# Kernel tuning notes

Hardware: AMD Instinct MI355X
Metric: run time of the kernel (lower is better)

The kernel has to match this reference:

```python
import jax, jax.numpy as jnp
import numpy as np
import math

SR = 24000
NH = 100      # num_harmonics
NF = 5        # num_formants
HID = 128
TWO_PI = 2.0 * math.pi


def conv1d(x, w, b, groups=1):
    # x: [B,C,T], w: [O, C//groups, K] (torch OIH layout), 'same' padding
    pad = (w.shape[-1] - 1) // 2
    y = jax.lax.conv_general_dilated(
        x, w, window_strides=(1,), padding=[(pad, pad)],
        dimension_numbers=('NCH', 'OIH', 'NCH'), feature_group_count=groups)
    return y + b[None, :, None]


def lrelu(x):
    return jnp.where(x >= 0, x, 0.1 * x)


def interp_linear(x, L):
    # torch F.interpolate(mode='linear', align_corners=False): x [B,C,T] -> [B,C,L]
    B, C, T = x.shape
    pos = (jnp.arange(L, dtype=x.dtype) + 0.5) * (T / L) - 0.5
    pos = jnp.clip(pos, 0.0, float(T - 1))
    lo = jnp.floor(pos).astype(jnp.int32)
    hi = jnp.minimum(lo + 1, T - 1)
    w = pos - lo.astype(x.dtype)
    return x[:, :, lo] * (1.0 - w) + x[:, :, hi] * w


def setup_inputs():
    key = jax.random.key(0)
    ks = jax.random.split(key, 30)
    ki = iter(range(30))
    def p(shape, s=0.05):
        return s * jax.random.normal(ks[next(ki)], shape, jnp.float32)
    B, T, L = 4, 500, 120000
    inp = {}
    # f0 in [80,120) Hz so actual_harmonics == num_harmonics (static shapes, see notes)
    inp['f0'] = 80.0 + 40.0 * jax.random.uniform(ks[next(ki)], (B, T), jnp.float32)
    inp['condition'] = jax.random.normal(ks[next(ki)], (B, HID, T), jnp.float32)
    # harmonic_amplitude_net params
    inp['ha_w1'] = p((HID, 1, 3));   inp['ha_b1'] = p((HID,))
    inp['ha_w2'] = p((256, HID, 1)); inp['ha_b2'] = p((256,))
    inp['ha_w3'] = p((256, 1, 3));   inp['ha_b3'] = p((256,))
    inp['ha_w4'] = p((256, 256, 1)); inp['ha_b4'] = p((256,))
    inp['ha_w5'] = p((NH, 256, 1));  inp['ha_b5'] = p((NH,))
    # formant predictor params
    inp['fm_w1'] = p((256, HID, 3));    inp['fm_b1'] = p((256,))
    inp['fm_w2'] = p((256, 256, 3));    inp['fm_b2'] = p((256,))
    inp['fm_w3'] = p((2 * NF, 256, 1)); inp['fm_b3'] = p((2 * NF,))
    # voice quality predictor params
    inp['vq_w1'] = p((128, HID, 3)); inp['vq_b1'] = p((128,))
    inp['vq_w2'] = p((64, 128, 3));  inp['vq_b2'] = p((64,))
    inp['vq_w3'] = p((3, 64, 1));    inp['vq_b3'] = p((3,))
    inp['audio_length'] = L
    return inp


def reference(f0, condition,
              ha_w1, ha_b1, ha_w2, ha_b2, ha_w3, ha_b3, ha_w4, ha_b4, ha_w5, ha_b5,
              fm_w1, fm_b1, fm_w2, fm_b2, fm_w3, fm_b3,
              vq_w1, vq_b1, vq_w2, vq_b2, vq_w3, vq_b3,
              audio_length):
    B, T = f0.shape
    L = audio_length
    # ---- harmonic_amplitude_net: (dw3 -> pw1 -> lrelu) x2 -> pw1 -> softplus ----
    a = lrelu(conv1d(conv1d(condition, ha_w1, ha_b1, groups=HID), ha_w2, ha_b2))
    a = lrelu(conv1d(conv1d(a, ha_w3, ha_b3, groups=256), ha_w4, ha_b4))
    harmonic_amplitudes = jax.nn.softplus(conv1d(a, ha_w5, ha_b5))  # [B,NH,T]
    # ---- FormantNetwork ----
    fp = conv1d(lrelu(conv1d(lrelu(conv1d(condition, fm_w1, fm_b1)), fm_w2, fm_b2)), fm_w3, fm_b3)
    ff = 200.0 + 3300.0 * jax.nn.sigmoid(fp[:, :NF])        # [B,NF,T]
    fbw = 50.0 + 150.0 * jax.nn.softplus(fp[:, NF:])        # [B,NF,T]
    hidx = jnp.arange(1, NH + 1, dtype=f0.dtype)
    hfreq = hidx[None, :, None] * f0[:, None, :]            # [B,NH,T]
    num = fbw ** 2                                          # [B,NF,T]
    den = (hfreq[:, None] - ff[:, :, None]) ** 2 + num[:, :, None]  # [B,NF,NH,T]
    res = num[:, :, None] / jnp.maximum(den, 1e-5)
    gain = jnp.prod(0.8 + 0.2 * res, axis=1)                # [B,NH,T]
    shaped = harmonic_amplitudes * gain
    # ---- VoiceQualityNetwork ----
    q = jax.nn.sigmoid(conv1d(lrelu(conv1d(lrelu(conv1d(condition, vq_w1, vq_b1)), vq_w2, vq_b2)), vq_w3, vq_b3))
    q_up = interp_linear(q, L)                              # [B,3,L]
    jitter = q_up[:, 0] * 0.05
    shimmer = q_up[:, 1] * 0.15
    breath = q_up[:, 2] * 0.3
    # ---- phase integration + harmonic bank ----
    f0_up = interp_linear(f0[:, None, :], L)[:, 0]          # [B,L]
    phase = jnp.cumsum(TWO_PI * f0_up / SR, axis=1)
    nk1, nk2, nk3 = jax.random.split(jax.random.key(42), 3)
    jphase = phase + jitter * jax.random.normal(nk1, phase.shape, phase.dtype)
    mask = (hidx[None, :, None] * f0_up[:, None, :] < SR / 2).astype(f0.dtype)  # [B,NH,L]
    amps_up = interp_linear(shaped, L)                      # [B,NH,L]
    sig = jnp.sum(amps_up * jnp.sin(jphase[:, None, :] * hidx[None, :, None]) * mask, axis=1)
    # ---- voice qualities: shimmer envelope + breath noise ----
    shim_env = 1.0 + jax.random.normal(nk2, sig.shape, sig.dtype) * shimmer
    out = sig * shim_env + jax.random.normal(nk3, sig.shape, sig.dtype) * breath
    return out
```

## Files before the change

kernel.cpp:

```cpp
#include <hip/hip_runtime.h>
#include <stdint.h>

#define B_ 4
#define T_ 500
#define L_ 120000
#define NH_ 100
#define N1_ 7500
#define N2_ 469
#define N2P_ 7504
#define N3_ 30
#define N3P_ 480
#define N4_ 2
#define N4P_ 32

#define ACT_NONE 0
#define ACT_LRELU 1
#define ACT_SOFTPLUS 2
#define ACT_SIGMOID 3

#define CH3 32
#define SXW3 132

__host__ __device__ __forceinline__ uint32_t tf_rotl(uint32_t v, int d) {
  return (v << d) | (v >> (32 - d));
}
__host__ __device__ __forceinline__ void tf_block(uint32_t k0, uint32_t k1,
                                                  uint32_t& x0, uint32_t& x1) {
  uint32_t k2 = k0 ^ k1 ^ 0x1BD11BDAu;
  x0 += k0; x1 += k1;
#define TF_R(d) x0 += x1; x1 = tf_rotl(x1, (d)); x1 ^= x0;
  TF_R(13) TF_R(15) TF_R(26) TF_R(6)   x0 += k1; x1 += k2 + 1u;
  TF_R(17) TF_R(29) TF_R(16) TF_R(24)  x0 += k2; x1 += k0 + 2u;
  TF_R(13) TF_R(15) TF_R(26) TF_R(6)   x0 += k0; x1 += k1 + 3u;
  TF_R(17) TF_R(29) TF_R(16) TF_R(24)  x0 += k1; x1 += k2 + 4u;
  TF_R(13) TF_R(15) TF_R(26) TF_R(6)   x0 += k2; x1 += k0 + 5u;
#undef TF_R
}

__device__ __forceinline__ float erfinv_xla(float x) {
  float w = -log1pf(-(x * x));
  float p;
  if (w < 5.0f) {
    w = w - 2.5f;
    p = 2.81022636e-08f;
    p = fmaf(p, w, 3.43273939e-07f);
    p = fmaf(p, w, -3.5233877e-06f);
    p = fmaf(p, w, -4.39150654e-06f);
    p = fmaf(p, w, 0.00021858087f);
    p = fmaf(p, w, -0.00125372503f);
    p = fmaf(p, w, -0.00417768164f);
    p = fmaf(p, w, 0.246640727f);
    p = fmaf(p, w, 1.50140941f);
  } else {
    w = sqrtf(w) - 3.0f;
    p = -0.000200214257f;
    p = fmaf(p, w, 0.000100950558f);
    p = fmaf(p, w, 0.00134934322f);
    p = fmaf(p, w, -0.00367342844f);
    p = fmaf(p, w, 0.00573950773f);
    p = fmaf(p, w, -0.0076224613f);
    p = fmaf(p, w, 0.00943887047f);
    p = fmaf(p, w, 1.00167406f);
    p = fmaf(p, w, 2.83297682f);
  }
  return p * x;
}

__device__ __forceinline__ float jax_normal(uint32_t k0, uint32_t k1, uint32_t e) {
  uint32_t x0 = 0u, x1 = e;
  tf_block(k0, k1, x0, x1);
  uint32_t bits = x0 ^ x1;
  float u = __uint_as_float((bits >> 9) | 0x3f800000u) - 1.0f;
  float v = __fadd_rn(__fmul_rn(u, 2.0f), -0x1.fffffep-1f);
  v = fmaxf(v, -0x1.fffffep-1f);
  return __fmul_rn((float)1.4142135623730951, erfinv_xla(v));
}

__device__ __forceinline__ float sin_acc(float xf) {
  double x = (double)xf;
  double kd = rint(x * 6.3661977236758138e-01);
  double r = fma(-kd, 1.5707963267948966e+00, x);
  r = fma(-kd, 6.1232339957367660e-17, r);
  float rf = (float)r;
  float y = rf * rf;
  float ps = fmaf(y, 2.7557319e-06f, -1.9841270e-04f);
  ps = fmaf(y, ps, 8.3333335e-03f);
  ps = fmaf(y, ps, -0.16666667f);
  float s = fmaf(rf * y, ps, rf);
  float pc = fmaf(y, -2.7557319e-07f, 2.4801587e-05f);
  pc = fmaf(y, pc, -1.3888889e-03f);
  pc = fmaf(y, pc, 4.1666668e-02f);
  pc = fmaf(y, pc, -0.5f);
  float c = fmaf(y, pc, 1.0f);
  int q = ((int)kd) & 3;
  float rs = (q & 1) ? c : s;
  return (q & 2) ? -rs : rs;
}

__device__ __forceinline__ float apply_act(float v, int act) {
  switch (act) {
    case ACT_LRELU:    return v >= 0.0f ? v : 0.1f * v;
    case ACT_SOFTPLUS: return fmaxf(v, 0.0f) + log1pf(expf(-fabsf(v)));
    case ACT_SIGMOID:  return 1.0f / (1.0f + expf(-v));
  }
  return v;
}


__device__ __forceinline__ void conv3_tile(
    const float* __restrict__ x, const float* __restrict__ w,
    const float* __restrict__ bias, float* __restrict__ y,
    int Cin, int Cout, int o0, int act, int b, int t0, float* smem) {
  float* sxf = smem;
  float* swf = smem + CH3 * SXW3;
  int tid = threadIdx.x;
  int lane = tid & 63, og = tid >> 6;
  int tl = 2 * lane;
  int t = t0 + tl;
  int obase = o0 + og * 4;
  float acc[4][2];
#pragma unroll
  for (int i = 0; i < 4; ++i) {
    float bv = (obase + i < Cout) ? bias[obase + i] : 0.0f;
    acc[i][0] = bv; acc[i][1] = bv;
  }
  float rx[17], rw[6];
  const int nch = Cin / CH3;
  auto ld = [&](int c) {
    int cb = c * CH3;
#pragma unroll
    for (int k = 0; k < 17; ++k) {
      int idx = tid + 256 * k;
      float v = 0.0f;
      if (idx < CH3 * 130) {
        int cc = idx / 130, j = idx - cc * 130;
        int tt = t0 - 1 + j;
        if (tt >= 0 && tt < T_) v = x[((size_t)b * Cin + cb + cc) * T_ + tt];
      }
      rx[k] = v;
    }
#pragma unroll
    for (int k = 0; k < 6; ++k) {
      int idx = tid + 256 * k;
      int oo = idx / 96, r = idx - oo * 96;
      rw[k] = (o0 + oo < Cout) ? w[((size_t)(o0 + oo) * Cin + cb) * 3 + r] : 0.0f;
    }
  };
  ld(0);
  for (int c = 0; c < nch; ++c) {
    __syncthreads();
#pragma unroll
    for (int k = 0; k < 17; ++k) {
      int idx = tid + 256 * k;
      if (idx < CH3 * 130) {
        int cc = idx / 130, j = idx - cc * 130;
        sxf[cc * SXW3 + j] = rx[k];
      }
    }
#pragma unroll
    for (int k = 0; k < 6; ++k) {
      int idx = tid + 256 * k;
      int oo = idx / 96, r = idx - oo * 96;
      swf[(r / 3) * 52 + oo * 3 + (r % 3)] = rw[k];
    }
    __syncthreads();
    if (c + 1 < nch) ld(c + 1);
    for (int cc = 0; cc < CH3; ++cc) {
      const float* row = sxf + cc * SXW3 + tl;
      float2 xa = *(const float2*)row;
      float2 xb = *(const float2*)(row + 2);
      const float4* wq = (const float4*)(swf + cc * 52 + og * 12);
      float4 W0 = wq[0], W1 = wq[1], W2 = wq[2];
      float wl[12] = {W0.x, W0.y, W0.z, W0.w, W1.x, W1.y, W1.z, W1.w,
                      W2.x, W2.y, W2.z, W2.w};
#pragma unroll
      for (int i = 0; i < 4; ++i) {
        float w0 = wl[3 * i], w1 = wl[3 * i + 1], w2 = wl[3 * i + 2];
        acc[i][0] = fmaf(xa.x, w0, acc[i][0]);
        acc[i][0] = fmaf(xa.y, w1, acc[i][0]);
        acc[i][0] = fmaf(xb.x, w2, acc[i][0]);
        acc[i][1] = fmaf(xa.y, w0, acc[i][1]);
        acc[i][1] = fmaf(xb.x, w1, acc[i][1]);
        acc[i][1] = fmaf(xb.y, w2, acc[i][1]);
      }
    }
  }
#pragma unroll
  for (int i = 0; i < 4; ++i) {
    int o = obase + i;
    if (o < Cout) {
      if (t < T_)     y[((size_t)b * Cout + o) * T_ + t]     = apply_act(acc[i][0], act);
      if (t + 1 < T_) y[((size_t)b * Cout + o) * T_ + t + 1] = apply_act(acc[i][1], act);
    }
  }
}

__device__ __forceinline__ void dwpw_tile(
    const float* __restrict__ x, const float* __restrict__ wd,
    const float* __restrict__ bd, const float* __restrict__ wp,
    const float* __restrict__ bp, float* __restrict__ y,
    int Cin, int Cout, int o0, int act, int b, int t0, float* smem) {
  float* sxf  = smem;
  float* swdf = smem + CH3 * SXW3;
  float* swpf = swdf + CH3 * 4;
  int tid = threadIdx.x;
  int lane = tid & 63, og = tid >> 6;
  int tl = 2 * lane;
  int t = t0 + tl;
  int obase = o0 + og * 4;
  float acc[4][2];
#pragma unroll
  for (int i = 0; i < 4; ++i) {
    float bv = (obase + i < Cout) ? bp[obase + i] : 0.0f;
    acc[i][0] = bv; acc[i][1] = bv;
  }
  float rx[17], rwp[2], rwd1 = 0.0f;
  const int nch = Cin / CH3;
  auto ld = [&](int c) {
    int cb = c * CH3;
#pragma unroll
    for (int k = 0; k < 17; ++k) {
      int idx = tid + 256 * k;
      float v = 0.0f;
      if (idx < CH3 * 130) {
        int cc = idx / 130, j = idx - cc * 130;
        int tt = t0 - 1 + j;
        if (tt >= 0 && tt < T_) v = x[((size_t)b * Cin + cb + cc) * T_ + tt];
      }
      rx[k] = v;
    }
    if (tid < CH3 * 4) {
      int cc = tid >> 2, q = tid & 3;
      rwd1 = (q < 3) ? wd[(size_t)(cb + cc) * 3 + q] : bd[cb + cc];
    }
#pragma unroll
    for (int k = 0; k < 2; ++k) {
      int idx = tid + 256 * k;
      int oo = idx >> 5, cc = idx & 31;
      rwp[k] = (o0 + oo < Cout) ? wp[(size_t)(o0 + oo) * Cin + cb + cc] : 0.0f;
    }
  };
  ld(0);
  for (int c = 0; c < nch; ++c) {
    __syncthreads();
#pragma unroll
    for (int k = 0; k < 17; ++k) {
      int idx = tid + 256 * k;
      if (idx < CH3 * 130) {
        int cc = idx / 130, j = idx - cc * 130;
        sxf[cc * SXW3 + j] = rx[k];
      }
    }
    if (tid < CH3 * 4) swdf[tid] = rwd1;
#pragma unroll
    for (int k = 0; k < 2; ++k) {
      int idx = tid + 256 * k;
      int oo = idx >> 5, cc = idx & 31;
      swpf[cc * 16 + oo] = rwp[k];
    }
    __syncthreads();
    if (c + 1 < nch) ld(c + 1);
    for (int cc = 0; cc < CH3; ++cc) {
      const float* row = sxf + cc * SXW3 + tl;
      float2 xa = *(const float2*)row;
      float2 xb = *(const float2*)(row + 2);
      float4 D = *(const float4*)(swdf + cc * 4);
      float d0 = fmaf(xa.x, D.x, fmaf(xa.y, D.y, fmaf(xb.x, D.z, D.w)));
      float d1 = fmaf(xa.y, D.x, fmaf(xb.x, D.y, fmaf(xb.y, D.z, D.w)));
      float4 Wp = *(const float4*)(swpf + cc * 16 + og * 4);
      acc[0][0] = fmaf(d0, Wp.x, acc[0][0]);
      acc[1][0] = fmaf(d0, Wp.y, acc[1][0]);
      acc[2][0] = fmaf(d0, Wp.z, acc[2][0]);
      acc[3][0] = fmaf(d0, Wp.w, acc[3][0]);
      acc[0][1] = fmaf(d1, Wp.x, acc[0][1]);
      acc[1][1] = fmaf(d1, Wp.y, acc[1][1]);
      acc[2][1] = fmaf(d1, Wp.z, acc[2][1]);
      acc[3][1] = fmaf(d1, Wp.w, acc[3][1]);
    }
  }
#pragma unroll
  for (int i = 0; i < 4; ++i) {
    int o = obase + i;
    if (o < Cout) {
      if (t < T_)     y[((size_t)b * Cout + o) * T_ + t]     = apply_act(acc[i][0], act);
      if (t + 1 < T_) y[((size_t)b * Cout + o) * T_ + t + 1] = apply_act(acc[i][1], act);
    }
  }
}

__device__ __forceinline__ void pw_stream(
    const float* __restrict__ x, const float* __restrict__ w,
    const float* __restrict__ bias, float* __restrict__ y,
    int Cin, int Cout, int o0, int act, int b, int t0, float* smem) {
  for (int idx = threadIdx.x; idx < 16 * Cin; idx += 256) {
    int oo = idx / Cin, cc = idx - oo * Cin;
    smem[cc * 16 + oo] = (o0 + oo < Cout) ? w[(size_t)(o0 + oo) * Cin + cc] : 0.0f;
  }
  __syncthreads();
  int lane = threadIdx.x & 63, og = threadIdx.x >> 6;
  int t = t0 + lane;
  int obase = o0 + og * 4;
  float acc[4];
#pragma unroll
  for (int i = 0; i < 4; ++i)
    acc[i] = (obase + i < Cout) ? bias[obase + i] : 0.0f;
  if (t < T_) {
    const float* xr = x + (size_t)b * Cin * T_ + t;
#pragma unroll 4
    for (int cc = 0; cc < Cin; ++cc) {
      float xv = xr[(size_t)cc * T_];
      float4 Wp = *(const float4*)(smem + cc * 16 + og * 4);
      acc[0] = fmaf(xv, Wp.x, acc[0]);
      acc[1] = fmaf(xv, Wp.y, acc[1]);
      acc[2] = fmaf(xv, Wp.z, acc[2]);
      acc[3] = fmaf(xv, Wp.w, acc[3]);
    }
#pragma unroll
    for (int i = 0; i < 4; ++i) {
      int o = obase + i;
      if (o < Cout) y[((size_t)b * Cout + o) * T_ + t] = apply_act(acc[i], act);
    }
  }
}

__device__ void terms_body(const float* __restrict__ f0, float* __restrict__ A1,
                           int base, int stride) {
  const float RINV = (float)(500.0 / 120000.0);
  for (int gid = base; gid < B_ * N1_; gid += stride) {
    int b = gid / N1_, w = gid - b * N1_;
    const float* f0b = f0 + (size_t)b * T_;
    float* a = A1 + (size_t)b * L_ + (size_t)w * 16;
    float S = 0.0f;
    int lbase = w * 16;
    for (int i = 0; i < 16; ++i) {
      int l = lbase + i;
      float pos = __fsub_rn(__fmul_rn(__fadd_rn((float)l, 0.5f), RINV), 0.5f);
      pos = fminf(fmaxf(pos, 0.0f), 499.0f);
      int lo = (int)floorf(pos);
      int hi = lo + 1; hi = hi < (T_ - 1) ? hi : (T_ - 1);
      float wt = __fsub_rn(pos, (float)lo);
      float omw = __fsub_rn(1.0f, wt);
      float f0up = __fadd_rn(__fmul_rn(f0b[lo], omw), __fmul_rn(f0b[hi], wt));
      float trm = __fdiv_rn(__fmul_rn((float)6.283185307179586, f0up), 24000.0f);
      S = __fadd_rn(S, trm);
      a[i] = S;
    }
  }
}

__device__ void rwr_body(const float* __restrict__ A1, float* __restrict__ A2,
                         float* __restrict__ A3, float* __restrict__ A4,
                         float* __restrict__ E5, float* __restrict__ E3o,
                         float* __restrict__ E2o) {
  int tid = threadIdx.x;
  for (int gid = tid; gid < B_ * N2_; gid += 256) {
    int b = gid / N2_, w = gid - b * N2_;
    float S = 0.0f;
    for (int m = 0; m < 16; ++m) {
      int i = w * 16 + m;
      float v = (i < N1_) ? A1[(size_t)b * L_ + (size_t)i * 16 + 15] : 0.0f;
      S = __fadd_rn(S, v);
      A2[(size_t)b * N2P_ + i] = S;
    }
  }
  __syncthreads();
  for (int gid = tid; gid < B_ * N3_; gid += 256) {
    int b = gid / N3_, w = gid - b * N3_;
    float S = 0.0f;
    for (int m = 0; m < 16; ++m) {
      int i = w * 16 + m;
      float v = (i < N2_) ? A2[(size_t)b * N2P_ + (size_t)i * 16 + 15] : 0.0f;
      S = __fadd_rn(S, v);
      A3[(size_t)b * N3P_ + i] = S;
    }
  }
  __syncthreads();
  for (int gid = tid; gid < B_ * N4_; gid += 256) {
    int b = gid / N4_, w = gid - b * N4_;
    float S = 0.0f;
    for (int m = 0; m < 16; ++m) {
      int i = w * 16 + m;
      float v = (i < N3_) ? A3[(size_t)b * N3P_ + (size_t)i * 16 + 15] : 0.0f;
      S = __fadd_rn(S, v);
      A4[(size_t)b * N4P_ + i] = S;
    }
  }
  __syncthreads();
  if (tid < B_) {
    E5[tid * N4_ + 0] = 0.0f;
    E5[tid * N4_ + 1] = A4[(size_t)tid * N4P_ + 15];
  }
  __syncthreads();
  for (int gid = tid; gid < B_ * N3_; gid += 256) {
    int b = gid / N3_, k = gid - b * N3_;
    float v = 0.0f;
    if (k > 0) {
      int i = k - 1;
      v = __fadd_rn(E5[b * N4_ + (i >> 4)], A4[(size_t)b * N4P_ + i]);
    }
    E3o[b * N3_ + k] = v;
  }
  __syncthreads();
  for (int gid = tid; gid < B_ * N2_; gid += 256) {
    int b = gid / N2_, j = gid - b * N2_;
    float v = 0.0f;
    if (j > 0) {
      int i = j - 1;
      v = __fadd_rn(E3o[b * N3_ + (i >> 4)], A3[(size_t)b * N3P_ + i]);
    }
    E2o[b * N2_ + j] = v;
  }
}

__global__ void __launch_bounds__(256) conv_l1(
    const float* __restrict__ cond, const float* __restrict__ f0,
    const float* __restrict__ fw1, const float* __restrict__ fb1,
    const float* __restrict__ vw1, const float* __restrict__ vb1,
    const float* __restrict__ hw1, const float* __restrict__ hb1,
    const float* __restrict__ hw2, const float* __restrict__ hb2,
    float* __restrict__ fmA, float* __restrict__ vqB, float* __restrict__ haB,
    float* __restrict__ A1) {
  __shared__ __align__(16) float smem[CH3 * SXW3 + CH3 * 52];
  int yy = blockIdx.y, b = blockIdx.z, t0 = blockIdx.x * 128;
  if (yy < 16) {
    conv3_tile(cond, fw1, fb1, fmA, 128, 256, yy * 16, ACT_LRELU, b, t0, smem);
  } else if (yy < 24) {
    conv3_tile(cond, vw1, vb1, vqB, 128, 128, (yy - 16) * 16, ACT_LRELU, b, t0, smem);
  } else if (yy < 40) {
    dwpw_tile(cond, hw1, hb1, hw2, hb2, haB, 128, 256, (yy - 24) * 16, ACT_LRELU, b, t0, smem);
  } else {
    int base = (blockIdx.z * 4 + blockIdx.x) * 256 + threadIdx.x;
    terms_body(f0, A1, base, 4096);
  }
}

__global__ void __launch_bounds__(256) conv_l2(
    const float* __restrict__ fmA, const float* __restrict__ vqB,
    const float* __restrict__ haB,
    const float* __restrict__ fw2, const float* __restrict__ fb2,
    const float* __restrict__ vw2, const float* __restrict__ vb2,
    const float* __restrict__ hw3, const float* __restrict__ hb3,
    const float* __restrict__ hw4, const float* __restrict__ hb4,
    float* __restrict__ fmC, float* __restrict__ vqC, float* __restrict__ haC,
    const float* __restrict__ A1, float* __restrict__ A2, float* __restrict__ A3,
    float* __restrict__ A4, float* __restrict__ E5, float* __restrict__ E3o,
    float* __restrict__ E2o) {
  __shared__ __align__(16) float smem[CH3 * SXW3 + CH3 * 52];
  int yy = blockIdx.y, b = blockIdx.z, t0 = blockIdx.x * 128;
  if (yy < 16) {
    conv3_tile(fmA, fw2, fb2, fmC, 256, 256, yy * 16, ACT_LRELU, b, t0, smem);
  } else if (yy < 20) {
    conv3_tile(vqB, vw2, vb2, vqC, 128, 64, (yy - 16) * 16, ACT_LRELU, b, t0, smem);
  } else if (yy < 36) {
    dwpw_tile(haB, hw3, hb3, hw4, hb4, haC, 256, 256, (yy - 20) * 16, ACT_LRELU, b, t0, smem);
  } else {
    if (blockIdx.x != 0 || blockIdx.z != 0) return;
    rwr_body(A1, A2, A3, A4, E5, E3o, E2o);
  }
}

__global__ void __launch_bounds__(256) conv_l3(
    const float* __restrict__ haC, const float* __restrict__ fmC,
    const float* __restrict__ vqC,
    const float* __restrict__ hw5, const float* __restrict__ hb5,
    const float* __restrict__ fw3, const float* __restrict__ fb3,
    const float* __restrict__ vw3, const float* __restrict__ vb3,
    float* __restrict__ ha, float* __restrict__ fp, float* __restrict__ qv) {
  __shared__ __align__(16) float smem[4096];
  int yy = blockIdx.y, b = blockIdx.z, t0 = blockIdx.x * 64;
  if (yy < 7) {
    pw_stream(haC, hw5, hb5, ha, 256, 100, yy * 16, ACT_SOFTPLUS, b, t0, smem);
  } else if (yy == 7) {
    pw_stream(fmC, fw3, fb3, fp, 256, 10, 0, ACT_NONE, b, t0, smem);
  } else {
    pw_stream(vqC, vw3, vb3, qv, 64, 3, 0, ACT_SIGMOID, b, t0, smem);
  }
}

__global__ void shaped_kernel(const float* __restrict__ ha, const float* __restrict__ fp,
                              const float* __restrict__ f0, float* __restrict__ out) {
  int t = blockIdx.x, b = blockIdx.y, h = threadIdx.x;
  __shared__ float ff[5], nm[5];
  if (h < 10) {
    float v = fp[((size_t)b * 10 + h) * T_ + t];
    if (h < 5) {
      ff[h] = 200.0f + 3300.0f * (1.0f / (1.0f + expf(-v)));
    } else {
      float bw = 50.0f + 150.0f * (fmaxf(v, 0.0f) + log1pf(expf(-fabsf(v))));
      nm[h - 5] = bw * bw;
    }
  }
  __syncthreads();
  if (h >= NH_) return;
  float hfreq = (float)(h + 1) * f0[(size_t)b * T_ + t];
  float g = 1.0f;
  for (int i = 0; i < 5; ++i) {
    float d = hfreq - ff[i];
    float den = d * d + nm[i];
    float res = nm[i] / fmaxf(den, 1e-5f);
    g = g * (0.8f + 0.2f * res);
  }
  out[((size_t)b * NH_ + h) * T_ + t] = ha[((size_t)b * NH_ + h) * T_ + t] * g;
}

__global__ void __launch_bounds__(256) main_kernel(
    const float* __restrict__ A1, const float* __restrict__ A2,
    const float* __restrict__ E2o,
    const float* __restrict__ shaped, const float* __restrict__ q,
    const float* __restrict__ f0, float* __restrict__ out,
    uint32_t k10, uint32_t k11, uint32_t k20, uint32_t k21, uint32_t k30, uint32_t k31) {
  const float RINV = (float)(500.0 / 120000.0);
  int b = blockIdx.y;
  int l0 = blockIdx.x * 256;
  int l = l0 + threadIdx.x;
  __shared__ float ls[4][NH_];
  float p0 = __fsub_rn(__fmul_rn(__fadd_rn((float)l0, 0.5f), RINV), 0.5f);
  p0 = fminf(fmaxf(p0, 0.0f), 499.0f);
  int lo0 = (int)floorf(p0);
  for (int i = threadIdx.x; i < 4 * NH_; i += 256) {
    int j = i / NH_, h = i - j * NH_;
    int col = lo0 + j; col = col < (T_ - 1) ? col : (T_ - 1);
    ls[j][h] = shaped[((size_t)b * NH_ + h) * T_ + col];
  }
  __syncthreads();
  if (l >= L_) return;

  float pos = __fsub_rn(__fmul_rn(__fadd_rn((float)l, 0.5f), RINV), 0.5f);
  pos = fminf(fmaxf(pos, 0.0f), 499.0f);
  int lo = (int)floorf(pos);
  int hi = lo + 1; hi = hi < (T_ - 1) ? hi : (T_ - 1);
  float w = __fsub_rn(pos, (float)lo);
  float omw = __fsub_rn(1.0f, w);

  const float* f0b = f0 + (size_t)b * T_;
  float f0up = __fadd_rn(__fmul_rn(f0b[lo], omw), __fmul_rn(f0b[hi], w));
  const float* qb = q + (size_t)b * 3 * T_;
  float q0 = __fadd_rn(__fmul_rn(qb[lo], omw), __fmul_rn(qb[hi], w));
  float q1 = __fadd_rn(__fmul_rn(qb[T_ + lo], omw), __fmul_rn(qb[T_ + hi], w));
  float q2 = __fadd_rn(__fmul_rn(qb[2 * T_ + lo], omw), __fmul_rn(qb[2 * T_ + hi], w));
  float jit = __fmul_rn(q0, 0.05f);
  float shm = __fmul_rn(q1, 0.15f);
  float brt = __fmul_rn(q2, 0.3f);

  uint32_t e = (uint32_t)(b * L_ + l);
  float n1 = jax_normal(k10, k11, e);
  float n2 = jax_normal(k20, k21, e);
  float n3 = jax_normal(k30, k31, e);

  float e1v = 0.0f;
  int r = l >> 4;
  if (r > 0) {
    int i = r - 1;
    e1v = __fadd_rn(E2o[b * N2_ + (i >> 4)], A2[(size_t)b * N2P_ + i]);
  }
  float phf = __fadd_rn(e1v, A1[(size_t)b * L_ + l]);
  float jph = __fadd_rn(phf, __fmul_rn(jit, n1));

  int jlo = lo - lo0;
  int jhi = hi - lo0; jhi = jhi < 3 ? jhi : 3;

  float acc = 0.0f;
  for (int h = 1; h <= NH_; ++h) {
    float amp = __fadd_rn(__fmul_rn(ls[jlo][h - 1], omw), __fmul_rn(ls[jhi][h - 1], w));
    float hf = (float)h;
    float arg = __fmul_rn(jph, hf);
    float s = sin_acc(arg);
    float m = (__fmul_rn(hf, f0up) < 12000.0f) ? 1.0f : 0.0f;
    acc = __fadd_rn(acc, __fmul_rn(__fmul_rn(amp, s), m));
  }
  float env = __fadd_rn(1.0f, __fmul_rn(n2, shm));
  out[(size_t)b * L_ + l] = __fadd_rn(__fmul_rn(acc, env), __fmul_rn(n3, brt));
}

extern "C" void kernel_launch(void* const* d_in, const int* in_sizes, int n_in,
                              void* d_out, int out_size, void* d_ws, size_t ws_size,
                              hipStream_t stream) {
  const float* f0    = (const float*)d_in[0];
  const float* cond  = (const float*)d_in[1];
  const float* ha_w1 = (const float*)d_in[2];
  const float* ha_b1 = (const float*)d_in[3];
  const float* ha_w2 = (const float*)d_in[4];
  const float* ha_b2 = (const float*)d_in[5];
  const float* ha_w3 = (const float*)d_in[6];
  const float* ha_b3 = (const float*)d_in[7];
  const float* ha_w4 = (const float*)d_in[8];
  const float* ha_b4 = (const float*)d_in[9];
  const float* ha_w5 = (const float*)d_in[10];
  const float* ha_b5 = (const float*)d_in[11];
  const float* fm_w1 = (const float*)d_in[12];
  const float* fm_b1 = (const float*)d_in[13];
  const float* fm_w2 = (const float*)d_in[14];
  const float* fm_b2 = (const float*)d_in[15];
  const float* fm_w3 = (const float*)d_in[16];
  const float* fm_b3 = (const float*)d_in[17];
  const float* vq_w1 = (const float*)d_in[18];
  const float* vq_b1 = (const float*)d_in[19];
  const float* vq_w2 = (const float*)d_in[20];
  const float* vq_b2 = (const float*)d_in[21];
  const float* vq_w3 = (const float*)d_in[22];
  const float* vq_b3 = (const float*)d_in[23];
  float* out = (float*)d_out;

  uint32_t kw[3][2];
  for (uint32_t j = 0; j < 3; ++j) {
    uint32_t x0 = 0u, x1 = j;
    tf_block(0u, 42u, x0, x1);
    kw[j][0] = x0; kw[j][1] = x1;
  }

  float* ws = (float*)d_ws;
  size_t off = 0;
  auto take = [&](size_t n) { float* p = ws + off; off += (n + 3) & ~(size_t)3; return p; };
  float* fmA = take(512000);
  float* haB = take(512000);
  float* fmC = take(512000);
  float* haC = take(512000);
  float* vqB = take(256000);
  float* vqC = take(128000);
  float* A1  = take((size_t)B_ * L_);
  float* A2  = take((size_t)B_ * N2P_);
  float* A3  = take((size_t)B_ * N3P_);
  float* A4  = take((size_t)B_ * N4P_);
  float* E5  = take((size_t)B_ * N4_);
  float* E3o = take((size_t)B_ * N3_);
  float* E2o = take((size_t)B_ * N2_);
  float* ha = fmA;
  float* fp = vqB;
  float* qv = vqB + 20480;
  float* sh = haB;

  conv_l1<<<dim3(4, 41, B_), 256, 0, stream>>>(
      cond, f0, fm_w1, fm_b1, vq_w1, vq_b1, ha_w1, ha_b1, ha_w2, ha_b2,
      fmA, vqB, haB, A1);
  conv_l2<<<dim3(4, 37, B_), 256, 0, stream>>>(
      fmA, vqB, haB, fm_w2, fm_b2, vq_w2, vq_b2, ha_w3, ha_b3, ha_w4, ha_b4,
      fmC, vqC, haC, A1, A2, A3, A4, E5, E3o, E2o);
  conv_l3<<<dim3(8, 9, B_), 256, 0, stream>>>(
      haC, fmC, vqC, ha_w5, ha_b5, fm_w3, fm_b3, vq_w3, vq_b3, ha, fp, qv);
  shaped_kernel<<<dim3(T_, B_), 128, 0, stream>>>(ha, fp, f0, sh);
  main_kernel<<<dim3((L_ + 255) / 256, B_), 256, 0, stream>>>(
      A1, A2, E2o, sh, qv, f0, out,
      kw[0][0], kw[0][1], kw[1][0], kw[1][1], kw[2][0], kw[2][1]);
  (void)in_sizes; (void)n_in; (void)out_size; (void)ws_size;
}
```

Measured before the change: 278.1 us.

## Widen conv time tiles to 256 with 4 outputs per thread

Each thread of the conv3 and depthwise-pointwise tiles now computes four time steps instead of two, and the block time tile grows from 128 to 256, which halves the grid along time. The goal is more FMA work per shared-memory load of weights and inputs, fewer halo loads, and vectorized float4 stores. In exchange, register pressure rises (33 staging registers plus 16 accumulators), fewer blocks are launched, which could hurt occupancy, and the float4 output stores rely on row offsets staying 16-byte aligned. The terms-body work is re-indexed so it still covers the same range with half as many blocks.

```diff
diff --git a/kernel.cpp b/kernel.cpp
--- a/kernel.cpp
+++ b/kernel.cpp
@@ -19,7 +19,7 @@
 #define ACT_SIGMOID 3
 
 #define CH3 32
-#define SXW3 132
+#define SXW3 260
 
 __host__ __device__ __forceinline__ uint32_t tf_rotl(uint32_t v, int d) {
   return (v << d) | (v >> (32 - d));
@@ -115,25 +115,26 @@
   float* swf = smem + CH3 * SXW3;
   int tid = threadIdx.x;
   int lane = tid & 63, og = tid >> 6;
-  int tl = 2 * lane;
+  int tl = 4 * lane;
   int t = t0 + tl;
   int obase = o0 + og * 4;
-  float acc[4][2];
+  float acc[4][4];
 #pragma unroll
   for (int i = 0; i < 4; ++i) {
     float bv = (obase + i < Cout) ? bias[obase + i] : 0.0f;
-    acc[i][0] = bv; acc[i][1] = bv;
-  }
-  float rx[17], rw[6];
+#pragma unroll
+    for (int j = 0; j < 4; ++j) acc[i][j] = bv;
+  }
+  float rx[33], rw[6];
   const int nch = Cin / CH3;
   auto ld = [&](int c) {
     int cb = c * CH3;
 #pragma unroll
-    for (int k = 0; k < 17; ++k) {
+    for (int k = 0; k < 33; ++k) {
       int idx = tid + 256 * k;
       float v = 0.0f;
-      if (idx < CH3 * 130) {
-        int cc = idx / 130, j = idx - cc * 130;
+      if (idx < CH3 * 258) {
+        int cc = idx / 258, j = idx - cc * 258;
         int tt = t0 - 1 + j;
         if (tt >= 0 && tt < T_) v = x[((size_t)b * Cin + cb + cc) * T_ + tt];
       }
@@ -150,10 +151,10 @@
   for (int c = 0; c < nch; ++c) {
     __syncthreads();
 #pragma unroll
-    for (int k = 0; k < 17; ++k) {
-      int idx = tid + 256 * k;
-      if (idx < CH3 * 130) {
-        int cc = idx / 130, j = idx - cc * 130;
+    for (int k = 0; k < 33; ++k) {
+      int idx = tid + 256 * k;
+      if (idx < CH3 * 258) {
+        int cc = idx / 258, j = idx - cc * 258;
         sxf[cc * SXW3 + j] = rx[k];
       }
     }
@@ -167,8 +168,9 @@
     if (c + 1 < nch) ld(c + 1);
     for (int cc = 0; cc < CH3; ++cc) {
       const float* row = sxf + cc * SXW3 + tl;
-      float2 xa = *(const float2*)row;
-      float2 xb = *(const float2*)(row + 2);
+      float4 X0 = *(const float4*)row;
+      float2 X1 = *(const float2*)(row + 4);
+      float xw[6] = {X0.x, X0.y, X0.z, X0.w, X1.x, X1.y};
       const float4* wq = (const float4*)(swf + cc * 52 + og * 12);
       float4 W0 = wq[0], W1 = wq[1], W2 = wq[2];
       float wl[12] = {W0.x, W0.y, W0.z, W0.w, W1.x, W1.y, W1.z, W1.w,
@@ -176,12 +178,12 @@
 #pragma unroll
       for (int i = 0; i < 4; ++i) {
         float w0 = wl[3 * i], w1 = wl[3 * i + 1], w2 = wl[3 * i + 2];
-        acc[i][0] = fmaf(xa.x, w0, acc[i][0]);
-        acc[i][0] = fmaf(xa.y, w1, acc[i][0]);
-        acc[i][0] = fmaf(xb.x, w2, acc[i][0]);
-        acc[i][1] = fmaf(xa.y, w0, acc[i][1]);
-        acc[i][1] = fmaf(xb.x, w1, acc[i][1]);
-        acc[i][1] = fmaf(xb.y, w2, acc[i][1]);
+#pragma unroll
+        for (int j = 0; j < 4; ++j) {
+          acc[i][j] = fmaf(xw[j],     w0, acc[i][j]);
+          acc[i][j] = fmaf(xw[j + 1], w1, acc[i][j]);
+          acc[i][j] = fmaf(xw[j + 2], w2, acc[i][j]);
+        }
       }
     }
   }
@@ -189,8 +191,15 @@
   for (int i = 0; i < 4; ++i) {
     int o = obase + i;
     if (o < Cout) {
-      if (t < T_)     y[((size_t)b * Cout + o) * T_ + t]     = apply_act(acc[i][0], act);
-      if (t + 1 < T_) y[((size_t)b * Cout + o) * T_ + t + 1] = apply_act(acc[i][1], act);
+      float* yp = y + ((size_t)b * Cout + o) * T_ + t;
+      if (t + 4 <= T_) {
+        *(float4*)yp = make_float4(apply_act(acc[i][0], act), apply_act(acc[i][1], act),
+                                   apply_act(acc[i][2], act), apply_act(acc[i][3], act));
+      } else {
+#pragma unroll
+        for (int j = 0; j < 4; ++j)
+          if (t + j < T_) yp[j] = apply_act(acc[i][j], act);
+      }
     }
   }
 }
@@ -205,25 +214,26 @@
   float* swpf = swdf + CH3 * 4;
   int tid = threadIdx.x;
   int lane = tid & 63, og = tid >> 6;
-  int tl = 2 * lane;
+  int tl = 4 * lane;
   int t = t0 + tl;
   int obase = o0 + og * 4;
-  float acc[4][2];
+  float acc[4][4];
 #pragma unroll
   for (int i = 0; i < 4; ++i) {
     float bv = (obase + i < Cout) ? bp[obase + i] : 0.0f;
-    acc[i][0] = bv; acc[i][1] = bv;
-  }
-  float rx[17], rwp[2], rwd1 = 0.0f;
+#pragma unroll
+    for (int j = 0; j < 4; ++j) acc[i][j] = bv;
+  }
+  float rx[33], rwp[2], rwd1 = 0.0f;
   const int nch = Cin / CH3;
   auto ld = [&](int c) {
     int cb = c * CH3;
 #pragma unroll
-    for (int k = 0; k < 17; ++k) {
+    for (int k = 0; k < 33; ++k) {
       int idx = tid + 256 * k;
       float v = 0.0f;
-      if (idx < CH3 * 130) {
-        int cc = idx / 130, j = idx - cc * 130;
+      if (idx < CH3 * 258) {
+        int cc = idx / 258, j = idx - cc * 258;
         int tt = t0 - 1 + j;
         if (tt >= 0 && tt < T_) v = x[((size_t)b * Cin + cb + cc) * T_ + tt];
       }
@@ -244,10 +254,10 @@
   for (int c = 0; c < nch; ++c) {
     __syncthreads();
 #pragma unroll
-    for (int k = 0; k < 17; ++k) {
-      int idx = tid + 256 * k;
-      if (idx < CH3 * 130) {
-        int cc = idx / 130, j = idx - cc * 130;
+    for (int k = 0; k < 33; ++k) {
+      int idx = tid + 256 * k;
+      if (idx < CH3 * 258) {
+        int cc = idx / 258, j = idx - cc * 258;
         sxf[cc * SXW3 + j] = rx[k];
       }
     }
@@ -262,28 +272,36 @@
     if (c + 1 < nch) ld(c + 1);
     for (int cc = 0; cc < CH3; ++cc) {
       const float* row = sxf + cc * SXW3 + tl;
-      float2 xa = *(const float2*)row;
-      float2 xb = *(const float2*)(row + 2);
+      float4 X0 = *(const float4*)row;
+      float2 X1 = *(const float2*)(row + 4);
+      float xw[6] = {X0.x, X0.y, X0.z, X0.w, X1.x, X1.y};
       float4 D = *(const float4*)(swdf + cc * 4);
-      float d0 = fmaf(xa.x, D.x, fmaf(xa.y, D.y, fmaf(xb.x, D.z, D.w)));
-      float d1 = fmaf(xa.y, D.x, fmaf(xb.x, D.y, fmaf(xb.y, D.z, D.w)));
+      float d[4];
+#pragma unroll
+      for (int j = 0; j < 4; ++j)
+        d[j] = fmaf(xw[j], D.x, fmaf(xw[j + 1], D.y, fmaf(xw[j + 2], D.z, D.w)));
       float4 Wp = *(const float4*)(swpf + cc * 16 + og * 4);
-      acc[0][0] = fmaf(d0, Wp.x, acc[0][0]);
-      acc[1][0] = fmaf(d0, Wp.y, acc[1][0]);
-      acc[2][0] = fmaf(d0, Wp.z, acc[2][0]);
-      acc[3][0] = fmaf(d0, Wp.w, acc[3][0]);
-      acc[0][1] = fmaf(d1, Wp.x, acc[0][1]);
-      acc[1][1] = fmaf(d1, Wp.y, acc[1][1]);
-      acc[2][1] = fmaf(d1, Wp.z, acc[2][1]);
-      acc[3][1] = fmaf(d1, Wp.w, acc[3][1]);
+      float wl[4] = {Wp.x, Wp.y, Wp.z, Wp.w};
+#pragma unroll
+      for (int i = 0; i < 4; ++i)
+#pragma unroll
+        for (int j = 0; j < 4; ++j)
+          acc[i][j] = fmaf(d[j], wl[i], acc[i][j]);
     }
   }
 #pragma unroll
   for (int i = 0; i < 4; ++i) {
     int o = obase + i;
     if (o < Cout) {
-      if (t < T_)     y[((size_t)b * Cout + o) * T_ + t]     = apply_act(acc[i][0], act);
-      if (t + 1 < T_) y[((size_t)b * Cout + o) * T_ + t + 1] = apply_act(acc[i][1], act);
+      float* yp = y + ((size_t)b * Cout + o) * T_ + t;
+      if (t + 4 <= T_) {
+        *(float4*)yp = make_float4(apply_act(acc[i][0], act), apply_act(acc[i][1], act),
+                                   apply_act(acc[i][2], act), apply_act(acc[i][3], act));
+      } else {
+#pragma unroll
+        for (int j = 0; j < 4; ++j)
+          if (t + j < T_) yp[j] = apply_act(acc[i][j], act);
+      }
     }
   }
 }
@@ -421,7 +439,7 @@
     float* __restrict__ fmA, float* __restrict__ vqB, float* __restrict__ haB,
     float* __restrict__ A1) {
   __shared__ __align__(16) float smem[CH3 * SXW3 + CH3 * 52];
-  int yy = blockIdx.y, b = blockIdx.z, t0 = blockIdx.x * 128;
+  int yy = blockIdx.y, b = blockIdx.z, t0 = blockIdx.x * 256;
   if (yy < 16) {
     conv3_tile(cond, fw1, fb1, fmA, 128, 256, yy * 16, ACT_LRELU, b, t0, smem);
   } else if (yy < 24) {
@@ -429,8 +447,8 @@
   } else if (yy < 40) {
     dwpw_tile(cond, hw1, hb1, hw2, hb2, haB, 128, 256, (yy - 24) * 16, ACT_LRELU, b, t0, smem);
   } else {
-    int base = (blockIdx.z * 4 + blockIdx.x) * 256 + threadIdx.x;
-    terms_body(f0, A1, base, 4096);
+    int base = (blockIdx.z * 2 + blockIdx.x) * 256 + threadIdx.x;
+    terms_body(f0, A1, base, 2048);
   }
 }
 
@@ -446,7 +464,7 @@
     float* __restrict__ A4, float* __restrict__ E5, float* __restrict__ E3o,
     float* __restrict__ E2o) {
   __shared__ __align__(16) float smem[CH3 * SXW3 + CH3 * 52];
-  int yy = blockIdx.y, b = blockIdx.z, t0 = blockIdx.x * 128;
+  int yy = blockIdx.y, b = blockIdx.z, t0 = blockIdx.x * 256;
   if (yy < 16) {
     conv3_tile(fmA, fw2, fb2, fmC, 256, 256, yy * 16, ACT_LRELU, b, t0, smem);
   } else if (yy < 20) {
@@ -629,10 +647,10 @@
   float* qv = vqB + 20480;
   float* sh = haB;
 
-  conv_l1<<<dim3(4, 41, B_), 256, 0, stream>>>(
+  conv_l1<<<dim3(2, 41, B_), 256, 0, stream>>>(
       cond, f0, fm_w1, fm_b1, vq_w1, vq_b1, ha_w1, ha_b1, ha_w2, ha_b2,
       fmA, vqB, haB, A1);
-  conv_l2<<<dim3(4, 37, B_), 256, 0, stream>>>(
+  conv_l2<<<dim3(2, 37, B_), 256, 0, stream>>>(
       fmA, vqB, haB, fm_w2, fm_b2, vq_w2, vq_b2, ha_w3, ha_b3, ha_w4, ha_b4,
       fmC, vqC, haC, A1, A2, A3, A4, E5, E3o, E2o);
   conv_l3<<<dim3(8, 9, B_), 256, 0, stream>>>(
```

New measurement: 337.1 us. 1.21x slower.
